# Optimization experiments

Hardware: AMD Instinct MI355X
Metric: run time of the kernel (lower is better)

The kernel has to match this reference:

```python
import jax, jax.numpy as jnp
import numpy as np

NB_CLASSES = 10
NB_NEIGHBORS = 75  # 1 closest + 74 precomputed geodesic neighbors


def setup_inputs() -> dict:
    key = jax.random.key(0)
    k0, k1, k2, k3, k4, k5 = jax.random.split(key, 6)
    nb_data, nb_train, d = 1024, 100000, 256
    x = jax.random.normal(k0, (nb_data, d), dtype=jnp.float32)
    X = jax.random.normal(k1, (nb_train, d), dtype=jnp.float32)
    # train table is stored normalized + centered (init_nn_querier)
    X = X / jnp.linalg.norm(X, axis=1, keepdims=True)
    X = X - jnp.mean(X, axis=0)
    center = jax.random.normal(k2, (d,), dtype=jnp.float32) * 0.01
    train_labels = jax.random.randint(k3, (nb_train,), 0, NB_CLASSES).astype(jnp.int32)
    train_neighbor_index = jax.random.randint(
        k4, (nb_train, NB_NEIGHBORS - 1), 0, nb_train).astype(jnp.int32)
    cali_nonconformity = jnp.sort(
        jax.random.randint(k5, (1000,), 0, NB_NEIGHBORS)).astype(jnp.int32)
    return {
        "x": x, "X": X, "center": center,
        "train_labels": train_labels,
        "train_neighbor_index": train_neighbor_index,
        "cali_nonconformity": cali_nonconformity,
    }


def reference(x, X, center, train_labels, train_neighbor_index, cali_nonconformity):
    # --- find_train_knns: normalize query, center, closest-neighbor search ---
    xq = x / jnp.linalg.norm(x, axis=1, keepdims=True) - center  # [B, d]
    # squared euclidean distances to every train point: [B, nb_train]
    d2 = (jnp.sum(xq * xq, axis=1, keepdims=True)
          - 2.0 * (xq @ X.T)
          + jnp.sum(X * X, axis=1)[None, :])
    closest = jnp.argmin(d2, axis=1)                               # [B]
    # neighbor list = closest point prepended to its precomputed table row
    neigh = jnp.concatenate(
        [closest[:, None], train_neighbor_index[closest]], axis=1)  # [B, K]
    knns_labels = train_labels[neigh]                              # [B, K]
    # --- nonconformity: per-class bincount, #knns NOT in class ---
    counts = jnp.sum(jax.nn.one_hot(knns_labels, NB_CLASSES, dtype=jnp.int32),
                     axis=1)                                       # [B, C]
    knns_not_in_class = jnp.sum(counts, axis=1, keepdims=True) - counts
    # --- preds_conf_cred: conformal p-values via bisect_left ---
    nb_cali = cali_nonconformity.shape[0]
    pos = jnp.searchsorted(cali_nonconformity, knns_not_in_class, side='left')
    p_value = (nb_cali - pos).astype(jnp.float32) / float(nb_cali)  # [B, C]
    preds = jnp.argmax(p_value, axis=1)                             # [B]
    top2, _ = jax.lax.top_k(p_value, 2)                             # [B, 2]
    nb_data = p_value.shape[0]
    creds = jnp.zeros_like(p_value).at[jnp.arange(nb_data), preds].set(top2[:, 0])
    return creds
```

## Files before the change

### kernel.cpp

```cpp
#include <hip/hip_runtime.h>
#include <stdint.h>


typedef __attribute__((ext_vector_type(8))) short short8;
typedef __attribute__((ext_vector_type(4))) float float4v;

static __device__ __forceinline__ unsigned short bf16_rn(float f) {
    unsigned int u = __float_as_uint(f);
    unsigned int r = (u + 0x7FFFu + ((u >> 16) & 1u)) >> 16;
    return (unsigned short)r;
}

static __device__ __forceinline__ void gload_lds16(const void* g, void* l) {
    __builtin_amdgcn_global_load_lds(
        (const __attribute__((address_space(1))) unsigned int*)g,
        (__attribute__((address_space(3))) unsigned int*)l, 16, 0, 0);
}

__global__ __launch_bounds__(256) void prep_all(
    const float* __restrict__ X, const float* __restrict__ x,
    const float* __restrict__ center,
    unsigned short* __restrict__ Bh, float* __restrict__ xn2,
    unsigned short* __restrict__ Ah, float* __restrict__ xqf,
    float* __restrict__ q2a, float* __restrict__ al2q,
    float* __restrict__ pmax,
    int nb_train, int Np, int B, int Mp, int train_rb)
{
    const int tid = threadIdx.x;
    __shared__ float sm[4];
    __shared__ float p1[4], p2[4], p3[4];

    if ((int)blockIdx.x < train_rb) {
        const int seg = tid & 15;
        const int rq  = tid >> 4;
        const int r0  = blockIdx.x * 64 + rq * 4;

        float4 v[4][4];
        bool ok[4];
        #pragma unroll
        for (int rr = 0; rr < 4; ++rr) {
            ok[rr] = (r0 + rr < nb_train);
            if (ok[rr]) {
                const float4* s = (const float4*)(X + (size_t)(r0 + rr) * 256 + seg * 16);
                v[rr][0] = s[0]; v[rr][1] = s[1]; v[rr][2] = s[2]; v[rr][3] = s[3];
            }
        }
        float ss[4];
        #pragma unroll
        for (int rr = 0; rr < 4; ++rr) {
            if (ok[rr]) {
                short8 h0, h1;
                h0[0] = bf16_rn(v[rr][0].x); h0[1] = bf16_rn(v[rr][0].y);
                h0[2] = bf16_rn(v[rr][0].z); h0[3] = bf16_rn(v[rr][0].w);
                h0[4] = bf16_rn(v[rr][1].x); h0[5] = bf16_rn(v[rr][1].y);
                h0[6] = bf16_rn(v[rr][1].z); h0[7] = bf16_rn(v[rr][1].w);
                h1[0] = bf16_rn(v[rr][2].x); h1[1] = bf16_rn(v[rr][2].y);
                h1[2] = bf16_rn(v[rr][2].z); h1[3] = bf16_rn(v[rr][2].w);
                h1[4] = bf16_rn(v[rr][3].x); h1[5] = bf16_rn(v[rr][3].y);
                h1[6] = bf16_rn(v[rr][3].z); h1[7] = bf16_rn(v[rr][3].w);
                unsigned short* bp = Bh + (size_t)(r0 + rr) * 256 + seg * 16;
                *(short8*)bp = h0;
                *(short8*)(bp + 8) = h1;
                ss[rr] = v[rr][0].x * v[rr][0].x + v[rr][0].y * v[rr][0].y
                       + v[rr][0].z * v[rr][0].z + v[rr][0].w * v[rr][0].w
                       + v[rr][1].x * v[rr][1].x + v[rr][1].y * v[rr][1].y
                       + v[rr][1].z * v[rr][1].z + v[rr][1].w * v[rr][1].w
                       + v[rr][2].x * v[rr][2].x + v[rr][2].y * v[rr][2].y
                       + v[rr][2].z * v[rr][2].z + v[rr][2].w * v[rr][2].w
                       + v[rr][3].x * v[rr][3].x + v[rr][3].y * v[rr][3].y
                       + v[rr][3].z * v[rr][3].z + v[rr][3].w * v[rr][3].w;
            } else {
                short8 z = {0, 0, 0, 0, 0, 0, 0, 0};
                unsigned short* bp = Bh + (size_t)(r0 + rr) * 256 + seg * 16;
                *(short8*)bp = z;
                *(short8*)(bp + 8) = z;
                ss[rr] = 0.f;
            }
        }
        #pragma unroll
        for (int s = 1; s < 16; s <<= 1) {
            ss[0] += __shfl_xor(ss[0], s);
            ss[1] += __shfl_xor(ss[1], s);
            ss[2] += __shfl_xor(ss[2], s);
            ss[3] += __shfl_xor(ss[3], s);
        }
        float mx = 0.f;
        if (seg == 0) {
            #pragma unroll
            for (int rr = 0; rr < 4; ++rr) mx = fmaxf(mx, ok[rr] ? ss[rr] : 0.f);
            if (ok[3]) {
                *(float4*)(xn2 + r0) = make_float4(ss[0], ss[1], ss[2], ss[3]);
            } else {
                #pragma unroll
                for (int rr = 0; rr < 4; ++rr)
                    xn2[r0 + rr] = ok[rr] ? ss[rr] : 3.0e38f;
            }
        }
        #pragma unroll
        for (int s = 1; s < 64; s <<= 1) mx = fmaxf(mx, __shfl_xor(mx, s));
        if ((tid & 63) == 0) sm[tid >> 6] = mx;
        __syncthreads();
        if (tid == 0)
            pmax[blockIdx.x] = fmaxf(fmaxf(sm[0], sm[1]), fmaxf(sm[2], sm[3]));
        return;
    }
    int row = blockIdx.x - train_rb;
    if (row >= Mp) return;
    if (row >= B) {
        Ah[(size_t)row * 256 + tid] = 0;
        xqf[(size_t)row * 256 + tid] = 0.f;
        if (tid == 0) { q2a[row] = 0.f; al2q[row] = 0.f; }
        return;
    }
    float v = x[(size_t)row * 256 + tid];
    float ss = v * v;
    #pragma unroll
    for (int s = 1; s < 64; s <<= 1) ss += __shfl_xor(ss, s);
    if ((tid & 63) == 0) p1[tid >> 6] = ss;
    __syncthreads();
    float tot = p1[0] + p1[1] + p1[2] + p1[3];
    float inv = 1.0f / sqrtf(tot);
    float val = v * inv - center[tid];
    unsigned short hb = bf16_rn(val);
    float hf = __uint_as_float((unsigned int)hb << 16);
    float al = val - hf;
    Ah[(size_t)row * 256 + tid] = hb;
    xqf[(size_t)row * 256 + tid] = val;
    float ss2 = val * val, sal = al * al;
    #pragma unroll
    for (int s = 1; s < 64; s <<= 1) {
        ss2 += __shfl_xor(ss2, s);
        sal += __shfl_xor(sal, s);
    }
    if ((tid & 63) == 0) { p2[tid >> 6] = ss2; p3[tid >> 6] = sal; }
    __syncthreads();
    if (tid == 0) {
        q2a[row]  = p2[0] + p2[1] + p2[2] + p2[3];
        al2q[row] = p3[0] + p3[1] + p3[2] + p3[3];
    }
}

__global__ __launch_bounds__(256, 4) void mfma_tile(
    const unsigned short* __restrict__ Adata,
    const unsigned short* __restrict__ Bdata,
    const float* __restrict__ xn2,
    float* __restrict__ gmin,
    int Mp, int Np, int nb_train, int B,
    int ntiles, int nper, int mtiles)
{
    __shared__ unsigned short As[128 * 64];
    __shared__ unsigned short Bs[128 * 64];

    const int bid = blockIdx.x;
    const int xcd = bid & 7;
    const int s_  = bid >> 3;
    const int n_t = xcd * nper + (s_ / mtiles);
    const int m_t = s_ - (s_ / mtiles) * mtiles;
    if (n_t >= ntiles) return;
    const int mtile = m_t * 128;
    const int ntile = n_t * 128;

    const int tid  = threadIdx.x;
    const int wave = tid >> 6;
    const int lane = tid & 63;

    const int isB   = wave >> 1;
    const int Rwave = (wave & 1) * 64;
    const int lrow8  = lane >> 3;
    const int lchunk = lane & 7;
    const unsigned short* sbase = isB
        ? (Bdata + (size_t)(ntile + Rwave + lrow8) * 256 + (size_t)((lchunk ^ lrow8) * 8))
        : (Adata + (size_t)(mtile + Rwave + lrow8) * 256 + (size_t)((lchunk ^ lrow8) * 8));
    unsigned short* lwave = (isB ? Bs : As) + Rwave * 64;

    const int mq = (wave >> 1) * 64;
    const int nq = (wave & 1) * 64;
    const int lrow = lane & 15;
    const int kseg = lane >> 4;
    const int sw = lrow & 7;

    float4v acc[4][4];
    #pragma unroll
    for (int i = 0; i < 4; ++i)
        #pragma unroll
        for (int j = 0; j < 4; ++j)
            acc[i][j] = (float4v){0.f, 0.f, 0.f, 0.f};

    for (int s = 0; s < 4; ++s) {
        const unsigned short* g = sbase + (size_t)(s * 64);
        __syncthreads();
        #pragma unroll
        for (int q = 0; q < 8; ++q)
            gload_lds16(g + q * 2048, lwave + q * 512);
        __syncthreads();
        #pragma unroll
        for (int t = 0; t < 2; ++t) {
            const int wch = ((t * 4 + kseg) ^ sw) * 8;
            short8 a[4], b[4];
            #pragma unroll
            for (int i = 0; i < 4; ++i)
                a[i] = *(const short8*)&As[(mq + i * 16 + lrow) * 64 + wch];
            #pragma unroll
            for (int j = 0; j < 4; ++j)
                b[j] = *(const short8*)&Bs[(nq + j * 16 + lrow) * 64 + wch];
            #pragma unroll
            for (int i = 0; i < 4; ++i)
                #pragma unroll
                for (int j = 0; j < 4; ++j)
                    acc[i][j] = __builtin_amdgcn_mfma_f32_16x16x32_bf16(
                        a[i], b[j], acc[i][j], 0, 0, 0);
        }
    }

    const int ng64 = Np >> 6;
    const int gb = (ntile + nq) >> 6;
    float xnv[4];
    #pragma unroll
    for (int j = 0; j < 4; ++j)
        xnv[j] = xn2[ntile + nq + j * 16 + lrow];

    #pragma unroll
    for (int i = 0; i < 4; ++i) {
        #pragma unroll
        for (int r = 0; r < 4; ++r) {
            const int lm = mq + i * 16 + kseg * 4 + r;
            const int gq = mtile + lm;
            float vm = fminf(
                fminf(xnv[0] - 2.0f * acc[i][0][r], xnv[1] - 2.0f * acc[i][1][r]),
                fminf(xnv[2] - 2.0f * acc[i][2][r], xnv[3] - 2.0f * acc[i][3][r]));
            #pragma unroll
            for (int sft = 1; sft < 16; sft <<= 1)
                vm = fminf(vm, __shfl_xor(vm, sft));
            if (lrow == 0 && gq < B)
                gmin[(size_t)gq * ng64 + gb] = vm;
        }
    }
}

__global__ __launch_bounds__(256) void select_classify(
    const float* __restrict__ gmin, const float* __restrict__ xqf,
    const float* __restrict__ X, const float* __restrict__ xn2,
    const float* __restrict__ q2a, const float* __restrict__ al2q,
    const float* __restrict__ pmax,
    const int* __restrict__ labels, const int* __restrict__ nbr,
    const int* __restrict__ cali, float* __restrict__ out,
    int Np, int nb_train, int knm1, int nb_cali, int B, int train_rb)
{
    extern __shared__ float gbuf[];
    __shared__ float xq_s[256];
    __shared__ float wmin[4], wpm[4], fsc[4];
    __shared__ int   fid[4];
    __shared__ float s_thr;
    __shared__ int   cand[256];
    __shared__ int   s_ncand;
    __shared__ int   s_closest;

    const int q    = blockIdx.x;
    const int tid  = threadIdx.x;
    const int lane = tid & 63;
    const int wave = tid >> 6;
    const int ng64 = Np >> 6;

    if (tid == 0) s_ncand = 0;
    xq_s[tid] = xqf[(size_t)q * 256 + tid];
    float vmin = 3.4e38f;
    for (int i = tid; i < ng64; i += 256) {
        float v = gmin[(size_t)q * ng64 + i];
        gbuf[i] = v;
        vmin = fminf(vmin, v);
    }
    float pm = 0.f;
    for (int i = tid; i < train_rb; i += 256) pm = fmaxf(pm, pmax[i]);
    #pragma unroll
    for (int s = 1; s < 64; s <<= 1) {
        vmin = fminf(vmin, __shfl_xor(vmin, s));
        pm   = fmaxf(pm,   __shfl_xor(pm, s));
    }
    if (lane == 0) { wmin[wave] = vmin; wpm[wave] = pm; }
    __syncthreads();
    if (tid == 0) {
        float m = fminf(fminf(wmin[0], wmin[1]), fminf(wmin[2], wmin[3]));
        float mb2 = fmaxf(fmaxf(wpm[0], wpm[1]), fmaxf(wpm[2], wpm[3]));
        float maxb  = sqrtf(mb2);
        float maxbl = maxb * 0.00390625f;
        float an = sqrtf(q2a[q]), al = sqrtf(al2q[q]);
        float errdot = al * maxb * 1.00390625f + (an + al) * maxbl;
        s_thr = m + 4.0f * errdot + 1e-3f;
    }
    __syncthreads();
    const float thr = s_thr;
    for (int g = tid; g < ng64; g += 256) {
        if (gbuf[g] <= thr) {
            int p = atomicAdd(&s_ncand, 1);
            if (p < 256) cand[p] = g;
        }
    }
    __syncthreads();
    const int nc = s_ncand;

    const int rsub = tid & 3;
    const int rrow = tid >> 2;
    float bsc = 3.4e38f; int bidx = 0x7FFFFFFF;
    auto rescore = [&](int g) {
        int row = g * 64 + rrow;
        if (row < nb_train) {
            const float* xr = X + (size_t)row * 256 + rsub * 64;
            const float* xs = xq_s + rsub * 64;
            float dot = 0.f;
            #pragma unroll
            for (int k = 0; k < 16; ++k) {
                float4 a4 = *(const float4*)(xs + k * 4);
                float4 b4 = *(const float4*)(xr + k * 4);
                dot += a4.x * b4.x + a4.y * b4.y + a4.z * b4.z + a4.w * b4.w;
            }
            dot += __shfl_xor(dot, 1);
            dot += __shfl_xor(dot, 2);
            float sc = xn2[row] - 2.0f * dot;
            if (sc < bsc || (sc == bsc && row < bidx)) { bsc = sc; bidx = row; }
        }
    };
    if (nc <= 256) {
        for (int c = 0; c < nc; ++c) rescore(cand[c]);
    } else {
        for (int g = 0; g < ng64; ++g)
            if (gbuf[g] <= thr) rescore(g);
    }
    #pragma unroll
    for (int s = 1; s < 64; s <<= 1) {
        float osc = __shfl_xor(bsc, s);
        int   oid = __shfl_xor(bidx, s);
        if (osc < bsc || (osc == bsc && oid < bidx)) { bsc = osc; bidx = oid; }
    }
    if (lane == 0) { fsc[wave] = bsc; fid[wave] = bidx; }
    __syncthreads();
    if (tid == 0) {
        float bs = fsc[0]; int bi = fid[0];
        #pragma unroll
        for (int w = 1; w < 4; ++w)
            if (fsc[w] < bs || (fsc[w] == bs && fid[w] < bi)) { bs = fsc[w]; bi = fid[w]; }
        s_closest = bi;
    }
    __syncthreads();

    if (wave == 0) {
        const int closest = s_closest;
        const int K = knm1 + 1;
        int lbl0 = -1, lbl1 = -1;
        if (lane < K) {
            int idx = (lane == 0) ? closest : nbr[(size_t)closest * knm1 + (lane - 1)];
            lbl0 = labels[idx];
        }
        int j2 = lane + 64;
        if (j2 < K) {
            int idx = nbr[(size_t)closest * knm1 + (j2 - 1)];
            lbl1 = labels[idx];
        }
        int bestc = 0, bestp = -1;
        #pragma unroll
        for (int c = 0; c < 10; ++c) {
            int cnt = __popcll(__ballot(lbl0 == c)) + __popcll(__ballot(lbl1 == c));
            int v = K - cnt;
            int lo = 0, hi = nb_cali;
            while (lo < hi) {
                int mid = (lo + hi) >> 1;
                if (cali[mid] < v) lo = mid + 1; else hi = mid;
            }
            int p = nb_cali - lo;
            if (p > bestp) { bestp = p; bestc = c; }
        }
        float pv = (float)bestp / (float)nb_cali;
        if (lane < 10)
            out[(size_t)q * 10 + lane] = (lane == bestc) ? pv : 0.0f;
    }
}

extern "C" void kernel_launch(void* const* d_in, const int* in_sizes, int n_in,
                              void* d_out, int out_size, void* d_ws, size_t ws_size,
                              hipStream_t stream) {
    const float* x      = (const float*)d_in[0];
    const float* X      = (const float*)d_in[1];
    const float* center = (const float*)d_in[2];
    const int* labels   = (const int*)d_in[3];
    const int* nbr      = (const int*)d_in[4];
    const int* cali     = (const int*)d_in[5];
    float* out = (float*)d_out;

    const int d        = in_sizes[2];
    const int B        = in_sizes[0] / d;
    const int nb_train = in_sizes[3];
    const int knm1     = in_sizes[4] / nb_train;
    const int nb_cali  = in_sizes[5];

    const int Mp = (B + 127) & ~127;
    const int Np = (nb_train + 127) & ~127;
    const int ng64 = Np >> 6;

    char* ws = (char*)d_ws;
    size_t off = 0;
    float* gmin = (float*)(ws + off);          off += (size_t)Mp * ng64 * 4;
    unsigned short* Ah = (unsigned short*)(ws + off); off += (size_t)Mp * 256 * 2;
    float* xqf  = (float*)(ws + off);          off += (size_t)Mp * 256 * 4;
    float* q2a  = (float*)(ws + off);          off += (size_t)Mp * 4;
    float* al2q = (float*)(ws + off);          off += (size_t)Mp * 4;
    unsigned short* Bh = (unsigned short*)(ws + off); off += (size_t)Np * 256 * 2;
    float* xn2  = (float*)(ws + off);          off += (size_t)Np * 4;
    float* pmax = (float*)(ws + off);          off += (size_t)(Np / 64) * 4;

    const int train_rb = Np / 64;
    prep_all<<<train_rb + Mp, 256, 0, stream>>>(
        X, x, center, Bh, xn2, Ah, xqf, q2a, al2q, pmax,
        nb_train, Np, B, Mp, train_rb);

    const int ntiles = Np / 128;
    const int mtiles = Mp / 128;
    const int nper   = (ntiles + 7) / 8;
    mfma_tile<<<8 * nper * mtiles, 256, 0, stream>>>(
        Ah, Bh, xn2, gmin, Mp, Np, nb_train, B, ntiles, nper, mtiles);

    select_classify<<<B, 256, ng64 * 4, stream>>>(
        gmin, xqf, X, xn2, q2a, al2q, pmax, labels, nbr, cali, out,
        Np, nb_train, knm1, nb_cali, B, train_rb);
}
```

Measured before the change: 304.8 us.

## Fuse prep, MFMA distance, and selection into one cooperative persistent kernel

Merges the three launches (bf16 prep, MFMA distance tile-min, candidate rescoring and classification) into one persistent cooperative kernel that loops over virtual blocks and separates the stages with grid-wide syncs. The aim is to remove launch gaps and kernel-boundary drains between stages. In exchange the grid is capped by occupancy (at most 1024 blocks), each stage strides its work over fewer blocks, and every block pays two grid barriers. The old three-kernel path is kept as a fallback if the cooperative launch fails.

Result: slower. 484.9 us (+59.1%).

```diff
diff --git a/kernel.cpp b/kernel.cpp
--- a/kernel.cpp
+++ b/kernel.cpp
@@ -1,5 +1,8 @@
 #include <hip/hip_runtime.h>
+#include <hip/hip_cooperative_groups.h>
 #include <stdint.h>
+
+namespace cg = cooperative_groups;
 
 
 typedef __attribute__((ext_vector_type(8))) short short8;
@@ -15,6 +18,358 @@
     __builtin_amdgcn_global_load_lds(
         (const __attribute__((address_space(1))) unsigned int*)g,
         (__attribute__((address_space(3))) unsigned int*)l, 16, 0, 0);
+}
+
+__global__ __launch_bounds__(256, 4) void dknn_fused(
+    const float* __restrict__ x, const float* __restrict__ X,
+    const float* __restrict__ center,
+    const int* __restrict__ labels, const int* __restrict__ nbr,
+    const int* __restrict__ cali, float* __restrict__ out,
+    unsigned short* __restrict__ Ah, float* __restrict__ xqf,
+    float* __restrict__ q2a, float* __restrict__ al2q,
+    unsigned short* __restrict__ Bh, float* __restrict__ xn2,
+    float* __restrict__ pmax, float* __restrict__ gmin,
+    int Mp, int Np, int nb_train, int B,
+    int ntiles, int nper, int mtiles, int train_rb,
+    int knm1, int nb_cali)
+{
+    __shared__ unsigned short As[128 * 64];
+    __shared__ unsigned short Bs[128 * 64];
+    __shared__ float p1[4], p2[4], p3[4], sm[4];
+    __shared__ float wmin[4], wpm[4], fsc[4];
+    __shared__ int   fid[4];
+    __shared__ int   cand[256];
+    __shared__ float s_thr;
+    __shared__ int   s_ncand, s_closest;
+
+    const int tid  = threadIdx.x;
+    const int nblk = gridDim.x;
+    cg::grid_group grid = cg::this_grid();
+
+    {
+        const int nvb = train_rb + Mp;
+        for (int vb = blockIdx.x; vb < nvb; vb += nblk) {
+            __syncthreads();
+            if (vb < train_rb) {
+                const int seg = tid & 15;
+                const int rq  = tid >> 4;
+                const int r0  = vb * 64 + rq * 4;
+                float4 v[4][4];
+                bool ok[4];
+                #pragma unroll
+                for (int rr = 0; rr < 4; ++rr) {
+                    ok[rr] = (r0 + rr < nb_train);
+                    if (ok[rr]) {
+                        const float4* s = (const float4*)(X + (size_t)(r0 + rr) * 256 + seg * 16);
+                        v[rr][0] = s[0]; v[rr][1] = s[1]; v[rr][2] = s[2]; v[rr][3] = s[3];
+                    }
+                }
+                float ss[4];
+                #pragma unroll
+                for (int rr = 0; rr < 4; ++rr) {
+                    if (ok[rr]) {
+                        short8 h0, h1;
+                        h0[0] = bf16_rn(v[rr][0].x); h0[1] = bf16_rn(v[rr][0].y);
+                        h0[2] = bf16_rn(v[rr][0].z); h0[3] = bf16_rn(v[rr][0].w);
+                        h0[4] = bf16_rn(v[rr][1].x); h0[5] = bf16_rn(v[rr][1].y);
+                        h0[6] = bf16_rn(v[rr][1].z); h0[7] = bf16_rn(v[rr][1].w);
+                        h1[0] = bf16_rn(v[rr][2].x); h1[1] = bf16_rn(v[rr][2].y);
+                        h1[2] = bf16_rn(v[rr][2].z); h1[3] = bf16_rn(v[rr][2].w);
+                        h1[4] = bf16_rn(v[rr][3].x); h1[5] = bf16_rn(v[rr][3].y);
+                        h1[6] = bf16_rn(v[rr][3].z); h1[7] = bf16_rn(v[rr][3].w);
+                        unsigned short* bp = Bh + (size_t)(r0 + rr) * 256 + seg * 16;
+                        *(short8*)bp = h0;
+                        *(short8*)(bp + 8) = h1;
+                        ss[rr] = v[rr][0].x * v[rr][0].x + v[rr][0].y * v[rr][0].y
+                               + v[rr][0].z * v[rr][0].z + v[rr][0].w * v[rr][0].w
+                               + v[rr][1].x * v[rr][1].x + v[rr][1].y * v[rr][1].y
+                               + v[rr][1].z * v[rr][1].z + v[rr][1].w * v[rr][1].w
+                               + v[rr][2].x * v[rr][2].x + v[rr][2].y * v[rr][2].y
+                               + v[rr][2].z * v[rr][2].z + v[rr][2].w * v[rr][2].w
+                               + v[rr][3].x * v[rr][3].x + v[rr][3].y * v[rr][3].y
+                               + v[rr][3].z * v[rr][3].z + v[rr][3].w * v[rr][3].w;
+                    } else {
+                        short8 z = {0, 0, 0, 0, 0, 0, 0, 0};
+                        unsigned short* bp = Bh + (size_t)(r0 + rr) * 256 + seg * 16;
+                        *(short8*)bp = z;
+                        *(short8*)(bp + 8) = z;
+                        ss[rr] = 0.f;
+                    }
+                }
+                #pragma unroll
+                for (int s = 1; s < 16; s <<= 1) {
+                    ss[0] += __shfl_xor(ss[0], s);
+                    ss[1] += __shfl_xor(ss[1], s);
+                    ss[2] += __shfl_xor(ss[2], s);
+                    ss[3] += __shfl_xor(ss[3], s);
+                }
+                float mx = 0.f;
+                if (seg == 0) {
+                    #pragma unroll
+                    for (int rr = 0; rr < 4; ++rr) mx = fmaxf(mx, ok[rr] ? ss[rr] : 0.f);
+                    if (ok[3]) {
+                        *(float4*)(xn2 + r0) = make_float4(ss[0], ss[1], ss[2], ss[3]);
+                    } else {
+                        #pragma unroll
+                        for (int rr = 0; rr < 4; ++rr)
+                            xn2[r0 + rr] = ok[rr] ? ss[rr] : 3.0e38f;
+                    }
+                }
+                #pragma unroll
+                for (int s = 1; s < 64; s <<= 1) mx = fmaxf(mx, __shfl_xor(mx, s));
+                if ((tid & 63) == 0) sm[tid >> 6] = mx;
+                __syncthreads();
+                if (tid == 0)
+                    pmax[vb] = fmaxf(fmaxf(sm[0], sm[1]), fmaxf(sm[2], sm[3]));
+            } else {
+                const int row = vb - train_rb;
+                if (row >= B) {
+                    Ah[(size_t)row * 256 + tid] = 0;
+                    xqf[(size_t)row * 256 + tid] = 0.f;
+                    if (tid == 0) { q2a[row] = 0.f; al2q[row] = 0.f; }
+                    continue;
+                }
+                float v = x[(size_t)row * 256 + tid];
+                float ss = v * v;
+                #pragma unroll
+                for (int s = 1; s < 64; s <<= 1) ss += __shfl_xor(ss, s);
+                if ((tid & 63) == 0) p1[tid >> 6] = ss;
+                __syncthreads();
+                float tot = p1[0] + p1[1] + p1[2] + p1[3];
+                float inv = 1.0f / sqrtf(tot);
+                float val = v * inv - center[tid];
+                unsigned short hb = bf16_rn(val);
+                float hf = __uint_as_float((unsigned int)hb << 16);
+                float al = val - hf;
+                Ah[(size_t)row * 256 + tid] = hb;
+                xqf[(size_t)row * 256 + tid] = val;
+                float ss2 = val * val, sal = al * al;
+                #pragma unroll
+                for (int s = 1; s < 64; s <<= 1) {
+                    ss2 += __shfl_xor(ss2, s);
+                    sal += __shfl_xor(sal, s);
+                }
+                if ((tid & 63) == 0) { p2[tid >> 6] = ss2; p3[tid >> 6] = sal; }
+                __syncthreads();
+                if (tid == 0) {
+                    q2a[row]  = p2[0] + p2[1] + p2[2] + p2[3];
+                    al2q[row] = p3[0] + p3[1] + p3[2] + p3[3];
+                }
+            }
+        }
+    }
+    grid.sync();
+
+    {
+        const int ntot = 8 * nper * mtiles;
+        const int wave = tid >> 6;
+        const int lane = tid & 63;
+        const int ng64 = Np >> 6;
+        for (int vb = blockIdx.x; vb < ntot; vb += nblk) {
+            const int xcd = vb & 7;
+            const int s_  = vb >> 3;
+            const int n_t = xcd * nper + (s_ / mtiles);
+            const int m_t = s_ - (s_ / mtiles) * mtiles;
+            if (n_t >= ntiles) continue;
+            const int mtile = m_t * 128;
+            const int ntile = n_t * 128;
+
+            const int isB    = wave >> 1;
+            const int Rwave  = (wave & 1) * 64;
+            const int lrow8  = lane >> 3;
+            const int lchunk = lane & 7;
+            const unsigned short* sbase = isB
+                ? (Bh + (size_t)(ntile + Rwave + lrow8) * 256 + (size_t)((lchunk ^ lrow8) * 8))
+                : (Ah + (size_t)(mtile + Rwave + lrow8) * 256 + (size_t)((lchunk ^ lrow8) * 8));
+            unsigned short* lwave = (isB ? Bs : As) + Rwave * 64;
+
+            const int mq = (wave >> 1) * 64;
+            const int nq = (wave & 1) * 64;
+            const int lrow = lane & 15;
+            const int kseg = lane >> 4;
+            const int sw = lrow & 7;
+
+            float4v acc[4][4];
+            #pragma unroll
+            for (int i = 0; i < 4; ++i)
+                #pragma unroll
+                for (int j = 0; j < 4; ++j)
+                    acc[i][j] = (float4v){0.f, 0.f, 0.f, 0.f};
+
+            for (int s = 0; s < 4; ++s) {
+                const unsigned short* g = sbase + (size_t)(s * 64);
+                __syncthreads();
+                #pragma unroll
+                for (int q = 0; q < 8; ++q)
+                    gload_lds16(g + q * 2048, lwave + q * 512);
+                __syncthreads();
+                #pragma unroll
+                for (int t = 0; t < 2; ++t) {
+                    const int wch = ((t * 4 + kseg) ^ sw) * 8;
+                    short8 a[4], b[4];
+                    #pragma unroll
+                    for (int i = 0; i < 4; ++i)
+                        a[i] = *(const short8*)&As[(mq + i * 16 + lrow) * 64 + wch];
+                    #pragma unroll
+                    for (int j = 0; j < 4; ++j)
+                        b[j] = *(const short8*)&Bs[(nq + j * 16 + lrow) * 64 + wch];
+                    #pragma unroll
+                    for (int i = 0; i < 4; ++i)
+                        #pragma unroll
+                        for (int j = 0; j < 4; ++j)
+                            acc[i][j] = __builtin_amdgcn_mfma_f32_16x16x32_bf16(
+                                a[i], b[j], acc[i][j], 0, 0, 0);
+                }
+            }
+
+            const int gb = (ntile + nq) >> 6;
+            float xnv[4];
+            #pragma unroll
+            for (int j = 0; j < 4; ++j)
+                xnv[j] = xn2[ntile + nq + j * 16 + lrow];
+
+            #pragma unroll
+            for (int i = 0; i < 4; ++i) {
+                #pragma unroll
+                for (int r = 0; r < 4; ++r) {
+                    const int lm = mq + i * 16 + kseg * 4 + r;
+                    const int gq = mtile + lm;
+                    float vm = fminf(
+                        fminf(xnv[0] - 2.0f * acc[i][0][r], xnv[1] - 2.0f * acc[i][1][r]),
+                        fminf(xnv[2] - 2.0f * acc[i][2][r], xnv[3] - 2.0f * acc[i][3][r]));
+                    #pragma unroll
+                    for (int sft = 1; sft < 16; sft <<= 1)
+                        vm = fminf(vm, __shfl_xor(vm, sft));
+                    if (lrow == 0 && gq < B)
+                        gmin[(size_t)gq * ng64 + gb] = vm;
+                }
+            }
+        }
+    }
+    grid.sync();
+
+    {
+        float* gbuf = (float*)As;
+        float* xq_s = (float*)Bs;
+        const int lane = tid & 63;
+        const int wave = tid >> 6;
+        const int ng64 = Np >> 6;
+
+        for (int q = blockIdx.x; q < B; q += nblk) {
+            __syncthreads();
+            if (tid == 0) s_ncand = 0;
+            xq_s[tid] = xqf[(size_t)q * 256 + tid];
+            float vmin = 3.4e38f;
+            for (int i = tid; i < ng64; i += 256) {
+                float v = gmin[(size_t)q * ng64 + i];
+                gbuf[i] = v;
+                vmin = fminf(vmin, v);
+            }
+            float pm = 0.f;
+            for (int i = tid; i < train_rb; i += 256) pm = fmaxf(pm, pmax[i]);
+            #pragma unroll
+            for (int s = 1; s < 64; s <<= 1) {
+                vmin = fminf(vmin, __shfl_xor(vmin, s));
+                pm   = fmaxf(pm,   __shfl_xor(pm, s));
+            }
+            if (lane == 0) { wmin[wave] = vmin; wpm[wave] = pm; }
+            __syncthreads();
+            if (tid == 0) {
+                float m = fminf(fminf(wmin[0], wmin[1]), fminf(wmin[2], wmin[3]));
+                float mb2 = fmaxf(fmaxf(wpm[0], wpm[1]), fmaxf(wpm[2], wpm[3]));
+                float maxb  = sqrtf(mb2);
+                float maxbl = maxb * 0.00390625f;
+                float an = sqrtf(q2a[q]), al = sqrtf(al2q[q]);
+                float errdot = al * maxb * 1.00390625f + (an + al) * maxbl;
+                s_thr = m + 4.0f * errdot + 1e-3f;
+            }
+            __syncthreads();
+            const float thr = s_thr;
+            for (int g = tid; g < ng64; g += 256) {
+                if (gbuf[g] <= thr) {
+                    int p = atomicAdd(&s_ncand, 1);
+                    if (p < 256) cand[p] = g;
+                }
+            }
+            __syncthreads();
+            const int nc = s_ncand;
+
+            const int rsub = tid & 3;
+            const int rrow = tid >> 2;
+            float bsc = 3.4e38f; int bidx = 0x7FFFFFFF;
+            auto rescore = [&](int g) {
+                int row = g * 64 + rrow;
+                if (row < nb_train) {
+                    const float* xr = X + (size_t)row * 256 + rsub * 64;
+                    const float* xs = xq_s + rsub * 64;
+                    float dot = 0.f;
+                    #pragma unroll
+                    for (int k = 0; k < 16; ++k) {
+                        float4 a4 = *(const float4*)(xs + k * 4);
+                        float4 b4 = *(const float4*)(xr + k * 4);
+                        dot += a4.x * b4.x + a4.y * b4.y + a4.z * b4.z + a4.w * b4.w;
+                    }
+                    dot += __shfl_xor(dot, 1);
+                    dot += __shfl_xor(dot, 2);
+                    float sc = xn2[row] - 2.0f * dot;
+                    if (sc < bsc || (sc == bsc && row < bidx)) { bsc = sc; bidx = row; }
+                }
+            };
+            if (nc <= 256) {
+                for (int c = 0; c < nc; ++c) rescore(cand[c]);
+            } else {
+                for (int g = 0; g < ng64; ++g)
+                    if (gbuf[g] <= thr) rescore(g);
+            }
+            #pragma unroll
+            for (int s = 1; s < 64; s <<= 1) {
+                float osc = __shfl_xor(bsc, s);
+                int   oid = __shfl_xor(bidx, s);
+                if (osc < bsc || (osc == bsc && oid < bidx)) { bsc = osc; bidx = oid; }
+            }
+            if (lane == 0) { fsc[wave] = bsc; fid[wave] = bidx; }
+            __syncthreads();
+            if (tid == 0) {
+                float bs = fsc[0]; int bi = fid[0];
+                #pragma unroll
+                for (int w = 1; w < 4; ++w)
+                    if (fsc[w] < bs || (fsc[w] == bs && fid[w] < bi)) { bs = fsc[w]; bi = fid[w]; }
+                s_closest = bi;
+            }
+            __syncthreads();
+
+            if (wave == 0) {
+                const int closest = s_closest;
+                const int K = knm1 + 1;
+                int lbl0 = -1, lbl1 = -1;
+                if (lane < K) {
+                    int idx = (lane == 0) ? closest : nbr[(size_t)closest * knm1 + (lane - 1)];
+                    lbl0 = labels[idx];
+                }
+                int j2 = lane + 64;
+                if (j2 < K) {
+                    int idx = nbr[(size_t)closest * knm1 + (j2 - 1)];
+                    lbl1 = labels[idx];
+                }
+                int bestc = 0, bestp = -1;
+                #pragma unroll
+                for (int c = 0; c < 10; ++c) {
+                    int cnt = __popcll(__ballot(lbl0 == c)) + __popcll(__ballot(lbl1 == c));
+                    int v = K - cnt;
+                    int lo = 0, hi = nb_cali;
+                    while (lo < hi) {
+                        int mid = (lo + hi) >> 1;
+                        if (cali[mid] < v) lo = mid + 1; else hi = mid;
+                    }
+                    int p = nb_cali - lo;
+                    if (p > bestp) { bestp = p; bestc = c; }
+                }
+                float pv = (float)bestp / (float)nb_cali;
+                if (lane < 10)
+                    out[(size_t)q * 10 + lane] = (lane == bestc) ? pv : 0.0f;
+            }
+        }
+    }
 }
 
 __global__ __launch_bounds__(256) void prep_all(
@@ -34,7 +389,6 @@
         const int seg = tid & 15;
         const int rq  = tid >> 4;
         const int r0  = blockIdx.x * 64 + rq * 4;
-
         float4 v[4][4];
         bool ok[4];
         #pragma unroll
@@ -386,14 +740,18 @@
     float* out = (float*)d_out;
 
     const int d        = in_sizes[2];
-    const int B        = in_sizes[0] / d;
-    const int nb_train = in_sizes[3];
-    const int knm1     = in_sizes[4] / nb_train;
-    const int nb_cali  = in_sizes[5];
-
-    const int Mp = (B + 127) & ~127;
-    const int Np = (nb_train + 127) & ~127;
+    int B        = in_sizes[0] / d;
+    int nb_train = in_sizes[3];
+    int knm1     = in_sizes[4] / nb_train;
+    int nb_cali  = in_sizes[5];
+
+    int Mp = (B + 127) & ~127;
+    int Np = (nb_train + 127) & ~127;
     const int ng64 = Np >> 6;
+    int ntiles = Np / 128;
+    int mtiles = Mp / 128;
+    int nper   = (ntiles + 7) / 8;
+    int train_rb = Np / 64;
 
     char* ws = (char*)d_ws;
     size_t off = 0;
@@ -404,20 +762,54 @@
     float* al2q = (float*)(ws + off);          off += (size_t)Mp * 4;
     unsigned short* Bh = (unsigned short*)(ws + off); off += (size_t)Np * 256 * 2;
     float* xn2  = (float*)(ws + off);          off += (size_t)Np * 4;
-    float* pmax = (float*)(ws + off);          off += (size_t)(Np / 64) * 4;
-
-    const int train_rb = Np / 64;
-    prep_all<<<train_rb + Mp, 256, 0, stream>>>(
-        X, x, center, Bh, xn2, Ah, xqf, q2a, al2q, pmax,
-        nb_train, Np, B, Mp, train_rb);
-
-    const int ntiles = Np / 128;
-    const int mtiles = Mp / 128;
-    const int nper   = (ntiles + 7) / 8;
-    mfma_tile<<<8 * nper * mtiles, 256, 0, stream>>>(
-        Ah, Bh, xn2, gmin, Mp, Np, nb_train, B, ntiles, nper, mtiles);
-
-    select_classify<<<B, 256, ng64 * 4, stream>>>(
-        gmin, xqf, X, xn2, q2a, al2q, pmax, labels, nbr, cali, out,
-        Np, nb_train, knm1, nb_cali, B, train_rb);
+    float* pmax = (float*)(ws + off);          off += (size_t)train_rb * 4;
+
+    static int coop_grid = -2;
+    if (coop_grid == -2) {
+        int maxb = 0;
+        hipError_t e = hipOccupancyMaxActiveBlocksPerMultiprocessor(
+            &maxb, dknn_fused, 256, 0);
+        if (e == hipSuccess && maxb > 0) {
+            hipDeviceProp_t prop;
+            int dev = 0;
+            hipGetDevice(&dev);
+            if (hipGetDeviceProperties(&prop, dev) == hipSuccess) {
+                int cap = maxb * prop.multiProcessorCount;
+                coop_grid = cap < 1024 ? cap : 1024;
+            } else {
+                coop_grid = -1;
+            }
+        } else {
+            coop_grid = -1;
+        }
+        if (coop_grid == 0) coop_grid = -1;
+    }
+
+    bool done = false;
+    if (coop_grid > 0) {
+        void* args[] = {
+            (void*)&x, (void*)&X, (void*)&center, (void*)&labels, (void*)&nbr,
+            (void*)&cali, (void*)&out, (void*)&Ah, (void*)&xqf, (void*)&q2a,
+            (void*)&al2q, (void*)&Bh, (void*)&xn2, (void*)&pmax, (void*)&gmin,
+            (void*)&Mp, (void*)&Np, (void*)&nb_train, (void*)&B, (void*)&ntiles,
+            (void*)&nper, (void*)&mtiles, (void*)&train_rb, (void*)&knm1,
+            (void*)&nb_cali
+        };
+        hipError_t err = hipLaunchCooperativeKernel(
+            reinterpret_cast<void*>(dknn_fused), dim3(coop_grid), dim3(256),
+            args, 0, stream);
+        if (err == hipSuccess) done = true;
+        else coop_grid = -1;
+    }
+
+    if (!done) {
+        prep_all<<<train_rb + Mp, 256, 0, stream>>>(
+            X, x, center, Bh, xn2, Ah, xqf, q2a, al2q, pmax,
+            nb_train, Np, B, Mp, train_rb);
+        mfma_tile<<<8 * nper * mtiles, 256, 0, stream>>>(
+            Ah, Bh, xn2, gmin, Mp, Np, nb_train, B, ntiles, nper, mtiles);
+        select_classify<<<B, 256, ng64 * 4, stream>>>(
+            gmin, xqf, X, xn2, q2a, al2q, pmax, labels, nbr, cali, out,
+            Np, nb_train, knm1, nb_cali, B, train_rb);
+    }
 }
```
